# Performance work log

Measured on AMD Instinct MI355X. Metric: run time of the kernel, lower is better.

## Reference

```python
import jax, jax.numpy as jnp
import numpy as np

HEADS = 8
DIM_HEAD = 64
SCALE = DIM_HEAD ** -0.5
EPS = 1e-7


def setup_inputs() -> dict:
    key = jax.random.key(0)
    ks = jax.random.split(key, 7)
    b, n, m, d = 8, 1024, 1024, 512
    inner = HEADS * DIM_HEAD  # 512
    s = lambda fan_in: 1.0 / np.sqrt(fan_in)
    return {
        "x": jax.random.normal(ks[0], (b, n, d), jnp.float32),
        "context": jax.random.normal(ks[1], (b, m, d), jnp.float32),
        "Wq": jax.random.normal(ks[2], (inner, d), jnp.float32) * s(d),
        "Wk": jax.random.normal(ks[3], (inner, d), jnp.float32) * s(d),
        "Wv": jax.random.normal(ks[4], (inner, d), jnp.float32) * s(d),
        "Wo": jax.random.normal(ks[5], (d, inner), jnp.float32) * s(inner),
        "bo": jnp.zeros((d,), jnp.float32),
    }


def _split_heads(t):
    # [b, n, h*d] -> [b, h, n, d]
    b, n, hd = t.shape
    return t.reshape(b, n, HEADS, DIM_HEAD).transpose(0, 2, 1, 3)


def reference(x, context, Wq, Wk, Wv, Wo, bo):
    # Linear projections (torch Linear: y = x @ W.T)
    q = _split_heads(jnp.einsum('bnd,ed->bne', x, Wq))        # [b,h,n,dh]
    k = _split_heads(jnp.einsum('bmd,ed->bme', context, Wk))  # [b,h,m,dh]
    v = _split_heads(jnp.einsum('bmd,ed->bme', context, Wv))  # [b,h,m,dh]

    sim = jnp.einsum('bhid,bhjd->bhij', q, k) * SCALE          # [b,h,n,m]

    # 'slot' attention: softmax over query dim (i), renormalize over keys (j)
    attn = jax.nn.softmax(sim, axis=2)
    attn = attn / (attn.sum(axis=-1, keepdims=True) + EPS)

    out = jnp.einsum('bhij,bhjd->bhid', attn, v)               # [b,h,n,dh]
    b, h, n, dh = out.shape
    out = out.transpose(0, 2, 1, 3).reshape(b, n, h * dh)      # [b,n,inner]
    return jnp.einsum('bne,de->bnd', out, Wo) + bo
```

## Files before the change

### kernel.cpp

```cpp
#include <hip/hip_runtime.h>

typedef __attribute__((ext_vector_type(8))) short short8;
typedef __attribute__((ext_vector_type(4))) float f32x4;
typedef __attribute__((ext_vector_type(16))) float f32x16;
typedef __attribute__((ext_vector_type(4))) unsigned short ushort4v;
typedef __attribute__((ext_vector_type(4))) unsigned int u32x4;
typedef unsigned short u16;
typedef unsigned int u32;

#define NN 1024
#define DD 512
#define DH 64
#define EXP2C 0.18033688f


__device__ __forceinline__ u16 f2bf(float f) {
    unsigned u = __float_as_uint(f);
    u += 0x7fffu + ((u >> 16) & 1u);
    return (u16)(u >> 16);
}

__device__ __forceinline__ float fexp2(float x) {
    float r;
    asm("v_exp_f32 %0, %1" : "=v"(r) : "v"(x));
    return r;
}

__device__ __forceinline__ u32 cvtpk(float a, float b) {
    u32 r;
    asm("v_cvt_pk_bf16_f32 %0, %1, %2" : "=v"(r) : "v"(a), "v"(b));
    return r;
}

__device__ __forceinline__ void stage_gll(const char* src, char* dst) {
    __builtin_amdgcn_global_load_lds(
        (const __attribute__((address_space(1))) unsigned int*)src,
        (__attribute__((address_space(3))) unsigned int*)dst, 16, 0, 0);
}

__device__ __forceinline__ short8 lds_ld128(const char* base, int row, int colbyte) {
    int off = (row * 128 + colbyte) ^ ((row & 7) << 4);
    return *(const short8*)(base + off);
}

__device__ __forceinline__ void stage128x64(const u16* g, int ldRow, char* lds,
                                            int wid, int lane) {
#pragma unroll
    for (int r = 0; r < 4; ++r) {
        int cidx = (r * 4 + wid) * 64 + lane;
        int row  = cidx >> 3;
        int ch   = (cidx & 7) ^ (row & 7);
        stage_gll((const char*)(g + row * ldRow) + ch * 16, lds + (r * 4 + wid) * 1024);
    }
}

__device__ __forceinline__ int offF2(int il, int hh, int t) {
    int c0 = t * 2 + hh;
    return ((il >> 1) << 8) + ((il & 1) << 7) + ((c0 ^ ((il >> 1) & 7)) << 4);
}

__device__ __forceinline__ int offF4(int il, int hh, int m, int tc) {
    int c0 = tc * 2 + hh;
    int line = m * 8 + (il >> 2);
    int s16 = (((il & 3) << 2) + c0) ^ ((il >> 2) & 7);
    return line * 256 + (s16 << 4);
}

__global__ void f2bf_all(const float* __restrict__ x, const float* __restrict__ ctx,
                         const float* __restrict__ Wq, const float* __restrict__ Wk,
                         const float* __restrict__ Wv, const float* __restrict__ Wo,
                         u16* __restrict__ xb, u16* __restrict__ cb,
                         u16* __restrict__ wb) {
    int i = blockIdx.x * blockDim.x + threadIdx.x;
    const float* src;
    u16* dst;
    int off;
    if (i < 1048576)      { src = x;   dst = xb; off = i; }
    else if (i < 2097152) { src = ctx; dst = cb; off = i - 1048576; }
    else {
        int wi = i - 2097152;
        int which = wi >> 16;
        off = wi & 65535;
        dst = wb + (size_t)which * 262144;
        src = (which == 0) ? Wq : (which == 1) ? Wk : (which == 2) ? Wv : Wo;
    }
    float4 v = ((const float4*)src)[off];
    ushort4v o;
    o.x = f2bf(v.x); o.y = f2bf(v.y); o.z = f2bf(v.z); o.w = f2bf(v.w);
    *(ushort4v*)(dst + (size_t)off * 4) = o;
}

__global__ __launch_bounds__(256, 2) void gemm_qkv(
    const u16* __restrict__ xb, const u16* __restrict__ cb, const u16* __restrict__ wb,
    u16* __restrict__ qb, u16* __restrict__ kb, u16* __restrict__ vT)
{
    alignas(16) __shared__ char smem[65536];
    const int z = blockIdx.z;
    const u16* A = (z == 0) ? xb : cb;
    const u16* B = wb + (size_t)z * 262144;
    const int lane = threadIdx.x & 63;
    const int wid  = threadIdx.x >> 6;
    const int wr = wid >> 1, wc = wid & 1;
    const int n = blockIdx.x + 4 * blockIdx.y;
    const int L = (n & 7) * 32 + (n >> 3);
    const int rowBase = (L >> 2) * 128;
    const int colBase = (L & 3) * 128;
    const u16* Abase = A + (size_t)rowBase * DD;
    const u16* Bbase = B + (size_t)colBase * DD;

    f32x4 acc[4][4] = {};
    stage128x64(Abase, DD, smem, wid, lane);
    stage128x64(Bbase, DD, smem + 32768, wid, lane);
    for (int kt = 0; kt < 8; ++kt) {
        __syncthreads();
        char* curA = smem + (kt & 1) * 16384;
        char* curB = smem + 32768 + (kt & 1) * 16384;
        if (kt < 7) {
            stage128x64(Abase + (kt + 1) * 64, DD, smem + ((kt + 1) & 1) * 16384, wid, lane);
            stage128x64(Bbase + (kt + 1) * 64, DD, smem + 32768 + ((kt + 1) & 1) * 16384, wid, lane);
        }
#pragma unroll
        for (int kk = 0; kk < 2; ++kk) {
            const int cbb = kk * 64 + (lane >> 4) * 16;
            short8 af[4], bf[4];
#pragma unroll
            for (int m = 0; m < 4; ++m) af[m] = lds_ld128(curA, wr * 64 + m * 16 + (lane & 15), cbb);
#pragma unroll
            for (int q = 0; q < 4; ++q) bf[q] = lds_ld128(curB, wc * 64 + q * 16 + (lane & 15), cbb);
#pragma unroll
            for (int m = 0; m < 4; ++m) {
#pragma unroll
                for (int q = 0; q < 4; ++q)
                    acc[m][q] = __builtin_amdgcn_mfma_f32_16x16x32_bf16(af[m], bf[q], acc[m][q], 0, 0, 0);
            }
        }
    }
#pragma unroll
    for (int m = 0; m < 4; ++m) {
#pragma unroll
        for (int q = 0; q < 4; ++q) {
            const int r0 = rowBase + wr * 64 + m * 16 + ((lane >> 4) << 2);
            const int c  = colBase + wc * 64 + q * 16 + (lane & 15);
            if (z < 2) {
                u16* O = z ? kb : qb;
#pragma unroll
                for (int g = 0; g < 4; ++g) O[(size_t)(r0 + g) * DD + c] = f2bf(acc[m][q][g]);
            } else {
                ushort4v pk;
#pragma unroll
                for (int g = 0; g < 4; ++g) pk[g] = f2bf(acc[m][q][g]);
                *(ushort4v*)(vT + (size_t)c * 8192 + r0) = pk;
            }
        }
    }
}

__global__ __launch_bounds__(256, 2) void gemm_out(
    const u16* __restrict__ A, const u16* __restrict__ B,
    float* __restrict__ Out, const float* __restrict__ bias)
{
    alignas(16) __shared__ char smem[65536];
    const int lane = threadIdx.x & 63;
    const int wid  = threadIdx.x >> 6;
    const int wr = wid >> 1, wc = wid & 1;
    const int n = blockIdx.x + 4 * blockIdx.y;
    const int L = (n & 7) * 32 + (n >> 3);
    const int rowBase = (L >> 2) * 128;
    const int colBase = (L & 3) * 128;
    const u16* Abase = A + (size_t)rowBase * DD;
    const u16* Bbase = B + (size_t)colBase * DD;

    f32x4 acc[4][4] = {};
    stage128x64(Abase, DD, smem, wid, lane);
    stage128x64(Bbase, DD, smem + 32768, wid, lane);
    for (int kt = 0; kt < 8; ++kt) {
        __syncthreads();
        char* curA = smem + (kt & 1) * 16384;
        char* curB = smem + 32768 + (kt & 1) * 16384;
        if (kt < 7) {
            stage128x64(Abase + (kt + 1) * 64, DD, smem + ((kt + 1) & 1) * 16384, wid, lane);
            stage128x64(Bbase + (kt + 1) * 64, DD, smem + 32768 + ((kt + 1) & 1) * 16384, wid, lane);
        }
#pragma unroll
        for (int kk = 0; kk < 2; ++kk) {
            const int cbb = kk * 64 + (lane >> 4) * 16;
            short8 af[4], bf[4];
#pragma unroll
            for (int m = 0; m < 4; ++m) af[m] = lds_ld128(curA, wr * 64 + m * 16 + (lane & 15), cbb);
#pragma unroll
            for (int q = 0; q < 4; ++q) bf[q] = lds_ld128(curB, wc * 64 + q * 16 + (lane & 15), cbb);
#pragma unroll
            for (int m = 0; m < 4; ++m) {
#pragma unroll
                for (int q = 0; q < 4; ++q)
                    acc[m][q] = __builtin_amdgcn_mfma_f32_16x16x32_bf16(af[m], bf[q], acc[m][q], 0, 0, 0);
            }
        }
    }
#pragma unroll
    for (int m = 0; m < 4; ++m) {
#pragma unroll
        for (int q = 0; q < 4; ++q) {
            const int r0 = rowBase + wr * 64 + m * 16 + ((lane >> 4) << 2);
            const int c  = colBase + wc * 64 + q * 16 + (lane & 15);
            const float bb = bias[c];
#pragma unroll
            for (int g = 0; g < 4; ++g) Out[(size_t)(r0 + g) * DD + c] = acc[m][q][g] + bb;
        }
    }
}

__global__ __launch_bounds__(256, 4) void colsum_k(
    const u16* __restrict__ qb, const u16* __restrict__ kb, float* __restrict__ lic)
{
    alignas(16) __shared__ char smem[16384];
    __shared__ float cs[128];
    const int tid = threadIdx.x;
    const int lane = tid & 63, wid = tid >> 6;
    const int il = lane & 31, hh = lane >> 5;
    const int n = blockIdx.x + 16 * blockIdx.y;
    const int L = (n & 7) * 128 + (n >> 3);
    const int jg = L & 15, bh = L >> 4;
    const int b = bh >> 3, h = bh & 7;
    const int jbp = wid & 1, ih = wid >> 1;
    const int jbase = jg * 64 + jbp * 32;

    const u16* kRow = kb + (size_t)(b * NN + jbase + il) * DD + h * DH + hh * 8;
    short8 kf[4];
#pragma unroll
    for (int t = 0; t < 4; ++t) kf[t] = *(const short8*)(kRow + t * 16);

    const int line = tid >> 4, s15 = tid & 15;
    const int slot8 = (s15 & 7) ^ (line & 7);
    const u16* qg0 = qb + (size_t)(b * NN) * DD + h * DH;
    const char* pQ0 = (const char*)(qg0 + (size_t)(line * 2 + (s15 >> 3)) * DD) + slot8 * 16;
    const char* pQ1 = pQ0 + 512 * DD * 2;
    const int dstoff = tid * 16;

    auto stageQ = [&](char* buf, const char* q0, const char* q1) {
        stage_gll(q0, buf + dstoff);
        stage_gll(q1, buf + 4096 + dstoff);
    };

    int oq[4];
#pragma unroll
    for (int t = 0; t < 4; ++t) oq[t] = offF2(il, hh, t) + ih * 4096;

    float cp[16] = {};
    stageQ(smem, pQ0, pQ1);
    pQ0 += 32768; pQ1 += 32768;
    for (int p = 0; p < 16; ++p) {
        char* buf = smem + (p & 1) * 8192;
        __syncthreads();
        if (p < 15) {
            stageQ(smem + ((p + 1) & 1) * 8192, pQ0, pQ1);
            pQ0 += 32768; pQ1 += 32768;
        }
        short8 qf[4];
#pragma unroll
        for (int t = 0; t < 4; ++t) qf[t] = *(const short8*)(buf + oq[t]);
        f32x16 sa = {};
#pragma unroll
        for (int t = 0; t < 4; ++t)
            sa = __builtin_amdgcn_mfma_f32_32x32x16_bf16(kf[t], qf[t], sa, 0, 0, 0);
#pragma unroll
        for (int r = 0; r < 16; ++r) cp[r] += fexp2(sa[r] * EXP2C);
    }
#pragma unroll
    for (int r = 0; r < 16; ++r) {
        cp[r] += __shfl_xor(cp[r], 1);
        cp[r] += __shfl_xor(cp[r], 2);
        cp[r] += __shfl_xor(cp[r], 4);
        cp[r] += __shfl_xor(cp[r], 8);
        cp[r] += __shfl_xor(cp[r], 16);
    }
    if (il == 0) {
#pragma unroll
        for (int r = 0; r < 16; ++r) cs[(jbp * 2 + ih) * 32 + hh * 16 + r] = cp[r];
    }
    __syncthreads();
    if (tid < 64) {
        int jbp2 = tid >> 5, jj = tid & 31;
        int r = (jj & 3) | ((jj >> 3) << 2);
        int h2 = (jj >> 2) & 1;
        float s = cs[(jbp2 * 2 + 0) * 32 + h2 * 16 + r] + cs[(jbp2 * 2 + 1) * 32 + h2 * 16 + r];
        lic[(size_t)bh * NN + jg * 64 + tid] = -__log2f(s);
    }
}

__global__ __launch_bounds__(256, 4) void attn_k(
    const u16* __restrict__ qb, const u16* __restrict__ kb, const u16* __restrict__ vT,
    const float* __restrict__ lic, u16* __restrict__ ob)
{
    alignas(16) __shared__ char smem[36864];
    const int tid = threadIdx.x;
    const int lane = tid & 63, wid = tid >> 6;
    const int il = lane & 31, hh = lane >> 5;
    const int n = blockIdx.x + 16 * blockIdx.y;
    const int L = (n & 7) * 128 + (n >> 3);
    const int ig = L & 15, bh = L >> 4;
    const int b = bh >> 3, h = bh & 7;
    const int ibp = wid & 1, jh = wid >> 1;
    const int ibase = ig * 64 + ibp * 32;
    char* licLds = smem + 32768;

    const u16* qRow = qb + (size_t)(b * NN + ibase + il) * DD + h * DH + hh * 8;
    short8 qf[4];
#pragma unroll
    for (int t = 0; t < 4; ++t) qf[t] = *(const short8*)(qRow + t * 16);

    {
        float4 lv = *(const float4*)(lic + (size_t)bh * NN + tid * 4);
        *(float4*)(licLds + tid * 16) = lv;
    }

    const int line = tid >> 4, s15 = tid & 15;
    const int slot8 = (s15 & 7) ^ (line & 7);
    const int s16 = s15 ^ (line & 7);
    const u16* kg0 = kb + (size_t)(b * NN) * DD + h * DH;
    const u16* vg0 = vT + (size_t)h * DH * 8192 + b * NN;
    const char* pK0 = (const char*)(kg0 + (size_t)(line * 2 + (s15 >> 3)) * DD) + slot8 * 16;
    const char* pK1 = pK0 + 512 * DD * 2;
    const char* pV0 = (const char*)(vg0 + (size_t)(line * 4 + (s16 >> 2)) * 8192) + (s16 & 3) * 16;
    const char* pV1 = pV0 + 512 * 2;
    const int dstoff = tid * 16;

    auto stageKV = [&](char* buf, const char* k0, const char* k1,
                       const char* v0, const char* v1) {
        stage_gll(k0, buf + dstoff);
        stage_gll(k1, buf + 4096 + dstoff);
        stage_gll(v0, buf + 8192 + dstoff);
        stage_gll(v1, buf + 12288 + dstoff);
    };

    int ok[4], ov[2][2];
#pragma unroll
    for (int t = 0; t < 4; ++t) ok[t] = offF2(il, hh, t) + jh * 4096;
#pragma unroll
    for (int m = 0; m < 2; ++m)
#pragma unroll
        for (int tc = 0; tc < 2; ++tc) ov[m][tc] = offF4(il, hh, m, tc) + 8192 + jh * 4096;

    f32x16 oacc[2] = {};
    float rs4[4] = {0.f, 0.f, 0.f, 0.f};

    stageKV(smem, pK0, pK1, pV0, pV1);
    pK0 += 32768; pK1 += 32768; pV0 += 64; pV1 += 64;
    for (int p = 0; p < 16; ++p) {
        char* buf = smem + (p & 1) * 16384;
        __syncthreads();
        if (p < 15) {
            stageKV(smem + ((p + 1) & 1) * 16384, pK0, pK1, pV0, pV1);
            pK0 += 32768; pK1 += 32768; pV0 += 64; pV1 += 64;
        }
        const int jb = (jh * 16 + p) * 32;
        short8 kf[4];
#pragma unroll
        for (int t = 0; t < 4; ++t) kf[t] = *(const short8*)(buf + ok[t]);
        f32x16 sa = {};
#pragma unroll
        for (int t = 0; t < 4; ++t)
            sa = __builtin_amdgcn_mfma_f32_32x32x16_bf16(kf[t], qf[t], sa, 0, 0, 0);
        u32 pk[4][2];
#pragma unroll
        for (int s = 0; s < 4; ++s) {
            const float4 lc = *(const float4*)(licLds + ((jb + 8 * s + 4 * hh) << 2));
            const float p0 = fexp2(fmaf(sa[4 * s + 0], EXP2C, lc.x));
            const float p1 = fexp2(fmaf(sa[4 * s + 1], EXP2C, lc.y));
            const float p2 = fexp2(fmaf(sa[4 * s + 2], EXP2C, lc.z));
            const float p3 = fexp2(fmaf(sa[4 * s + 3], EXP2C, lc.w));
            rs4[s] += (p0 + p1) + (p2 + p3);
            pk[s][0] = cvtpk(p0, p1);
            pk[s][1] = cvtpk(p2, p3);
        }
        short8 vf[2][2];
#pragma unroll
        for (int m = 0; m < 2; ++m)
#pragma unroll
            for (int tc = 0; tc < 2; ++tc) vf[m][tc] = *(const short8*)(buf + ov[m][tc]);
#pragma unroll
        for (int tc = 0; tc < 2; ++tc) {
            int a0 = (int)pk[2 * tc][0], b0 = (int)pk[2 * tc + 1][0];
            int a1 = (int)pk[2 * tc][1], b1 = (int)pk[2 * tc + 1][1];
            asm("v_permlane32_swap_b32 %0, %1" : "+v"(a0), "+v"(b0));
            asm("v_permlane32_swap_b32 %0, %1" : "+v"(a1), "+v"(b1));
            u32x4 pw;
            pw.x = (u32)a0;
            pw.y = (u32)a1;
            pw.z = (u32)b0;
            pw.w = (u32)b1;
            const short8 pf = __builtin_bit_cast(short8, pw);
#pragma unroll
            for (int m = 0; m < 2; ++m)
                oacc[m] = __builtin_amdgcn_mfma_f32_32x32x16_bf16(vf[m][tc], pf, oacc[m], 0, 0, 0);
        }
    }

    float rs = (rs4[0] + rs4[1]) + (rs4[2] + rs4[3]);
    rs += __shfl_xor(rs, 32);
    __syncthreads();
    float* cO = (float*)smem;
    float* cR = (float*)(smem + 16384);
    if (jh == 1) {
#pragma unroll
        for (int m = 0; m < 2; ++m)
#pragma unroll
            for (int r = 0; r < 16; ++r) cO[(ibp * 32 + m * 16 + r) * 64 + lane] = oacc[m][r];
        cR[ibp * 64 + lane] = rs;
    }
    __syncthreads();
    if (jh == 0) {
#pragma unroll
        for (int m = 0; m < 2; ++m)
#pragma unroll
            for (int r = 0; r < 16; ++r) oacc[m][r] += cO[(ibp * 32 + m * 16 + r) * 64 + lane];
        rs += cR[ibp * 64 + lane];
        const float inv = 1.0f / (rs + 1e-7f);
        u16* oRow = ob + (size_t)(b * NN + ibase + il) * DD + h * DH;
#pragma unroll
        for (int m = 0; m < 2; ++m) {
#pragma unroll
            for (int s = 0; s < 4; ++s) {
                ushort4v st;
#pragma unroll
                for (int g = 0; g < 4; ++g) st[g] = f2bf(oacc[m][4 * s + g] * inv);
                *(ushort4v*)(oRow + m * 32 + 8 * s + 4 * hh) = st;
            }
        }
    }
}


extern "C" void kernel_launch(void* const* d_in, const int* in_sizes, int n_in,
                              void* d_out, int out_size, void* d_ws, size_t ws_size,
                              hipStream_t stream)
{
    (void)in_sizes; (void)n_in; (void)out_size; (void)ws_size;
    const float* x   = (const float*)d_in[0];
    const float* ctx = (const float*)d_in[1];
    const float* Wq  = (const float*)d_in[2];
    const float* Wk  = (const float*)d_in[3];
    const float* Wv  = (const float*)d_in[4];
    const float* Wo  = (const float*)d_in[5];
    const float* bo  = (const float*)d_in[6];
    float* out = (float*)d_out;

    char* w = (char*)d_ws;
    const size_t SZBIG = 8192ull * 512 * 2;
    u16* xb  = (u16*)(w);
    u16* cb  = (u16*)(w + SZBIG);
    u16* qb  = (u16*)(w + 2 * SZBIG);
    u16* kb  = (u16*)(w + 3 * SZBIG);
    u16* vT  = (u16*)(w + 4 * SZBIG);
    u16* wb  = (u16*)(w + 5 * SZBIG);
    u16* wob = wb + 3 * 262144;
    float* lic = (float*)(w + 5 * SZBIG + 4 * 524288);
    u16* ob = xb;

    f2bf_all<<<9216, 256, 0, stream>>>(x, ctx, Wq, Wk, Wv, Wo, xb, cb, wb);

    gemm_qkv<<<dim3(4, 64, 3), 256, 0, stream>>>(xb, cb, wb, qb, kb, vT);

    colsum_k<<<dim3(16, 64), 256, 0, stream>>>(qb, kb, lic);
    attn_k  <<<dim3(16, 64), 256, 0, stream>>>(qb, kb, vT, lic, ob);

    gemm_out<<<dim3(4, 64), 256, 0, stream>>>(ob, wob, out, bo);
}
```

Baseline: 86.94 us.

## Fuse fp32-to-bf16 activation conversion into QKV GEMM A-tile loading

Result: no change. 88.58 us (+1.9%).

```diff
diff --git a/kernel.cpp b/kernel.cpp
--- a/kernel.cpp
+++ b/kernel.cpp
@@ -4,6 +4,7 @@
 typedef __attribute__((ext_vector_type(4))) float f32x4;
 typedef __attribute__((ext_vector_type(16))) float f32x16;
 typedef __attribute__((ext_vector_type(4))) unsigned short ushort4v;
+typedef __attribute__((ext_vector_type(2))) unsigned int u32x2;
 typedef __attribute__((ext_vector_type(4))) unsigned int u32x4;
 typedef unsigned short u16;
 typedef unsigned int u32;
@@ -66,58 +67,72 @@
     return line * 256 + (s16 << 4);
 }
 
-__global__ void f2bf_all(const float* __restrict__ x, const float* __restrict__ ctx,
-                         const float* __restrict__ Wq, const float* __restrict__ Wk,
-                         const float* __restrict__ Wv, const float* __restrict__ Wo,
-                         u16* __restrict__ xb, u16* __restrict__ cb,
-                         u16* __restrict__ wb) {
+__global__ void f2bf_w(const float* __restrict__ Wq, const float* __restrict__ Wk,
+                       const float* __restrict__ Wv, const float* __restrict__ Wo,
+                       u16* __restrict__ wb) {
     int i = blockIdx.x * blockDim.x + threadIdx.x;
-    const float* src;
-    u16* dst;
-    int off;
-    if (i < 1048576)      { src = x;   dst = xb; off = i; }
-    else if (i < 2097152) { src = ctx; dst = cb; off = i - 1048576; }
-    else {
-        int wi = i - 2097152;
-        int which = wi >> 16;
-        off = wi & 65535;
-        dst = wb + (size_t)which * 262144;
-        src = (which == 0) ? Wq : (which == 1) ? Wk : (which == 2) ? Wv : Wo;
-    }
+    int which = i >> 16;
+    int off = i & 65535;
+    const float* src = (which == 0) ? Wq : (which == 1) ? Wk : (which == 2) ? Wv : Wo;
     float4 v = ((const float4*)src)[off];
     ushort4v o;
     o.x = f2bf(v.x); o.y = f2bf(v.y); o.z = f2bf(v.z); o.w = f2bf(v.w);
-    *(ushort4v*)(dst + (size_t)off * 4) = o;
+    *(ushort4v*)(wb + (size_t)which * 262144 + (size_t)off * 4) = o;
 }
 
 __global__ __launch_bounds__(256, 2) void gemm_qkv(
-    const u16* __restrict__ xb, const u16* __restrict__ cb, const u16* __restrict__ wb,
+    const float* __restrict__ x, const float* __restrict__ ctxp, const u16* __restrict__ wb,
     u16* __restrict__ qb, u16* __restrict__ kb, u16* __restrict__ vT)
 {
     alignas(16) __shared__ char smem[65536];
     const int z = blockIdx.z;
-    const u16* A = (z == 0) ? xb : cb;
+    const float* A = (z == 0) ? x : ctxp;
     const u16* B = wb + (size_t)z * 262144;
-    const int lane = threadIdx.x & 63;
-    const int wid  = threadIdx.x >> 6;
+    const int tid = threadIdx.x;
+    const int lane = tid & 63;
+    const int wid  = tid >> 6;
     const int wr = wid >> 1, wc = wid & 1;
     const int n = blockIdx.x + 4 * blockIdx.y;
     const int L = (n & 7) * 32 + (n >> 3);
     const int rowBase = (L >> 2) * 128;
     const int colBase = (L & 3) * 128;
-    const u16* Abase = A + (size_t)rowBase * DD;
     const u16* Bbase = B + (size_t)colBase * DD;
 
+    const int arow = tid >> 4;
+    const int acol4 = (tid & 15) * 4;
+    const float* Ath = A + (size_t)(rowBase + arow) * DD + acol4;
+    const int awbase = arow * 128 + (((tid & 15) * 8) ^ ((arow & 7) << 4));
+
     f32x4 acc[4][4] = {};
-    stage128x64(Abase, DD, smem, wid, lane);
+    float4 av[8];
+#pragma unroll
+    for (int i = 0; i < 8; ++i) av[i] = *(const float4*)(Ath + (size_t)i * 16 * DD);
+#pragma unroll
+    for (int i = 0; i < 8; ++i) {
+        u32x2 wv; wv.x = cvtpk(av[i].x, av[i].y); wv.y = cvtpk(av[i].z, av[i].w);
+        *(u32x2*)(smem + i * 2048 + awbase) = wv;
+    }
     stage128x64(Bbase, DD, smem + 32768, wid, lane);
+#pragma unroll
+    for (int i = 0; i < 8; ++i) av[i] = *(const float4*)(Ath + (size_t)i * 16 * DD + 64);
+
     for (int kt = 0; kt < 8; ++kt) {
         __syncthreads();
         char* curA = smem + (kt & 1) * 16384;
         char* curB = smem + 32768 + (kt & 1) * 16384;
         if (kt < 7) {
-            stage128x64(Abase + (kt + 1) * 64, DD, smem + ((kt + 1) & 1) * 16384, wid, lane);
             stage128x64(Bbase + (kt + 1) * 64, DD, smem + 32768 + ((kt + 1) & 1) * 16384, wid, lane);
+            char* altA = smem + ((kt + 1) & 1) * 16384;
+#pragma unroll
+            for (int i = 0; i < 8; ++i) {
+                u32x2 wv; wv.x = cvtpk(av[i].x, av[i].y); wv.y = cvtpk(av[i].z, av[i].w);
+                *(u32x2*)(altA + i * 2048 + awbase) = wv;
+            }
+            if (kt < 6) {
+#pragma unroll
+                for (int i = 0; i < 8; ++i)
+                    av[i] = *(const float4*)(Ath + (size_t)i * 16 * DD + (kt + 2) * 64);
+            }
         }
 #pragma unroll
         for (int kk = 0; kk < 2; ++kk) {
@@ -447,19 +462,17 @@
 
     char* w = (char*)d_ws;
     const size_t SZBIG = 8192ull * 512 * 2;
-    u16* xb  = (u16*)(w);
-    u16* cb  = (u16*)(w + SZBIG);
+    u16* ob  = (u16*)(w);
     u16* qb  = (u16*)(w + 2 * SZBIG);
     u16* kb  = (u16*)(w + 3 * SZBIG);
     u16* vT  = (u16*)(w + 4 * SZBIG);
     u16* wb  = (u16*)(w + 5 * SZBIG);
     u16* wob = wb + 3 * 262144;
     float* lic = (float*)(w + 5 * SZBIG + 4 * 524288);
-    u16* ob = xb;
-
-    f2bf_all<<<9216, 256, 0, stream>>>(x, ctx, Wq, Wk, Wv, Wo, xb, cb, wb);
-
-    gemm_qkv<<<dim3(4, 64, 3), 256, 0, stream>>>(xb, cb, wb, qb, kb, vT);
+
+    f2bf_w<<<1024, 256, 0, stream>>>(Wq, Wk, Wv, Wo, wb);
+
+    gemm_qkv<<<dim3(4, 64, 3), 256, 0, stream>>>(x, ctx, wb, qb, kb, vT);
 
     colsum_k<<<dim3(16, 64), 256, 0, stream>>>(qb, kb, lic);
     attn_k  <<<dim3(16, 64), 256, 0, stream>>>(qb, kb, vT, lic, ob);
```
